# Kernel optimization log

Hardware: AMD Instinct MI355X
Metric: run time of the kernel (lower is better)

Reference implementation:

```python
import jax, jax.numpy as jnp
import numpy as np


def conv2d_nchw(x, w, b, padding):
    # x: [B,Cin,H,W], w: [Cout,Cin,kh,kw]
    y = jax.lax.conv_general_dilated(
        x, w, window_strides=(1, 1), padding=padding,
        dimension_numbers=("NCHW", "OIHW", "NCHW"))
    return y + b[None, :, None, None]


def setup_inputs() -> dict:
    key = jax.random.key(0)
    ks = jax.random.split(key, 8)
    B, C, H, W = 8, 512, 50, 76
    A = 9  # 3 scales x 3 ratios
    base_feat = jax.random.normal(ks[0], (B, C, H, W), dtype=jnp.float32)
    im_info = jnp.tile(jnp.array([800.0, 1216.0, 1.0], jnp.float32), (B, 1))
    gt_boxes = jax.random.uniform(ks[1], (B, 20, 5), dtype=jnp.float32) * 100.0
    num_boxes = jax.random.randint(ks[2], (B,), 1, 20, dtype=jnp.int32)
    # learned parameters (Kaiming-ish small init)
    conv_w = jax.random.normal(ks[3], (512, C, 3, 3), dtype=jnp.float32) * 0.01
    conv_b = jnp.zeros((512,), jnp.float32)
    cls_w = jax.random.normal(ks[4], (2 * A, 512, 1, 1), dtype=jnp.float32) * 0.01
    cls_b = jnp.zeros((2 * A,), jnp.float32)
    bbox_w = jax.random.normal(ks[5], (4 * A, 512, 1, 1), dtype=jnp.float32) * 0.01
    bbox_b = jnp.zeros((4 * A,), jnp.float32)
    return dict(base_feat=base_feat, im_info=im_info, gt_boxes=gt_boxes,
                num_boxes=num_boxes, conv_w=conv_w, conv_b=conv_b,
                cls_w=cls_w, cls_b=cls_b, bbox_w=bbox_w, bbox_b=bbox_b)


def reference(base_feat, im_info, gt_boxes, num_boxes,
              conv_w, conv_b, cls_w, cls_b, bbox_w, bbox_b):
    # RPN_Conv 3x3 + ReLU
    rpn_conv = jax.nn.relu(conv2d_nchw(base_feat, conv_w, conv_b, "SAME"))
    # 1x1 cls head -> [B, 2A, H, W]
    rpn_cls_score = conv2d_nchw(rpn_conv, cls_w, cls_b, "VALID")
    B, C2, H, W = rpn_cls_score.shape
    # _RPN.reshape(x, 2): view as [B, 2, A*H, W], softmax over the 2-way dim
    score_rs = rpn_cls_score.reshape(B, 2, (C2 // 2) * H, W)
    prob_rs = jax.nn.softmax(score_rs, axis=1)
    rpn_cls_prob = prob_rs.reshape(B, C2, H, W)
    # 1x1 bbox head -> [B, 4A, H, W]
    rpn_bbox_pred = conv2d_nchw(rpn_conv, bbox_w, bbox_b, "VALID")
    return rpn_cls_prob, rpn_bbox_pred
```

## Files before the change

kernel.cpp:

```cpp
#include <hip/hip_runtime.h>
#include <hip/hip_bf16.h>


typedef __bf16 bf16_t;
typedef __attribute__((ext_vector_type(8))) __bf16 bf16x8;
typedef __attribute__((ext_vector_type(4))) __bf16 bf16x4;
typedef __attribute__((ext_vector_type(4))) float f32x4;

#define HW 3800
#define NPOS (8 * HW)
#define XP_IMG (52 * 78 * 512)

__device__ __forceinline__ void gload_lds16(const bf16_t* g, char* l) {
  __builtin_amdgcn_global_load_lds(
      (const __attribute__((address_space(1))) unsigned int*)g,
      (__attribute__((address_space(3))) unsigned int*)l, 16, 0, 0);
}

__global__ __launch_bounds__(256) void prep_all(const float* __restrict__ x,
                                                const float* __restrict__ cw,
                                                const float* __restrict__ clsw,
                                                const float* __restrict__ boxw,
                                                bf16_t* __restrict__ Xp,
                                                bf16_t* __restrict__ Wt,
                                                bf16_t* __restrict__ Whb) {
  __shared__ __align__(16) bf16_t tile[76][136];
  __shared__ bf16_t lw[4608];
  const int t = threadIdx.x;
  const int blk = blockIdx.x;
  if (blk < 1600) {
    const int cb = blk & 3;
    int r = blk >> 2;
    const int h = r % 50, b = r / 50;
#pragma unroll
    for (int it = 0; it < 10; ++it) {
      int idx = it * 256 + t;
      if (idx < 2432) {
        int c = idx / 19, w4 = idx - c * 19;
        const float4 v = *(const float4*)(x +
            (((size_t)(b * 512 + cb * 128 + c)) * 50 + h) * 76 + w4 * 4);
        tile[w4 * 4 + 0][c] = (bf16_t)v.x;
        tile[w4 * 4 + 1][c] = (bf16_t)v.y;
        tile[w4 * 4 + 2][c] = (bf16_t)v.z;
        tile[w4 * 4 + 3][c] = (bf16_t)v.w;
      }
    }
    __syncthreads();
#pragma unroll
    for (int it = 0; it < 5; ++it) {
      int idx = it * 256 + t;
      if (idx < 1216) {
        int w = idx >> 4, c8 = idx & 15;
        bf16x8 v = *(const bf16x8*)&tile[w][c8 * 8];
        *(bf16x8*)(Xp + ((size_t)(b * 52 + h + 1) * 78 + (w + 1)) * 512 +
                   cb * 128 + c8 * 8) = v;
      }
    }
  } else if (blk < 1616) {
    const int blk2 = blk - 1600;
    const int b = blk2 >> 1, half = blk2 & 1;
    bf16x8 z;
#pragma unroll
    for (int j = 0; j < 8; ++j) z[j] = (bf16_t)0.f;
#pragma unroll
    for (int it = 0; it < 32; ++it) {
      int idx = it * 256 + t;
      int q = half * 128 + (idx >> 6);
      int c8 = idx & 63;
      int h, w;
      if (q < 78)       { h = 0;           w = q; }
      else if (q < 156) { h = 51;          w = q - 78; }
      else if (q < 206) { h = q - 156 + 1; w = 0; }
      else              { h = q - 206 + 1; w = 77; }
      *(bf16x8*)(Xp + ((size_t)(b * 52 + h) * 78 + w) * 512 + c8 * 8) = z;
    }
  } else if (blk < 2128) {
    const int co = blk - 1616;
    const float* src = cw + (size_t)co * 4608;
#pragma unroll
    for (int it = 0; it < 18; ++it) {
      int idx = it * 256 + t;
      lw[idx] = (bf16_t)src[idx];
    }
    __syncthreads();
#pragma unroll
    for (int s = 0; s < 9; ++s) {
      int ci = t * 2;
      bf16_t v0 = lw[ci * 9 + s], v1 = lw[(ci + 1) * 9 + s];
      bf16_t* dst = Wt + ((size_t)s * 512 + co) * 512 + ci;
      dst[0] = v0; dst[1] = v1;
    }
  } else {
    int g = (blk - 2128) * 256 + t;
    int ci = g & 511; int row = g >> 9;
    float v = 0.f;
    if (row < 18) {
      int a = row >> 1, logit = row & 1;
      v = clsw[(logit * 9 + a) * 512 + ci];
    } else if (row < 54) {
      v = boxw[(row - 18) * 512 + ci];
    }
    Whb[(size_t)row * 512 + ci] = (bf16_t)v;
  }
}

__global__ __launch_bounds__(512) void conv3x3(const bf16_t* __restrict__ Xp,
                                               const bf16_t* __restrict__ Wt,
                                               const float* __restrict__ convb,
                                               bf16_t* __restrict__ rc2) {
  __shared__ __align__(16) char smem[131072];
  const int tid = threadIdx.x;
  const int lane = tid & 63;
  const int wv = tid >> 6;
  const int wm = wv >> 2;
  const int wn = wv & 3;
  const int lm = lane & 15, lg = lane >> 4;

  const int raw = blockIdx.x;
  const int wg = (raw & 7) * 30 + (raw >> 3);
  const int b = wg / 30;
  const int rem = wg - b * 30;
  const int co_base = (rem & 1) * 256;
  const int pos_base = (rem >> 1) * 256;

  int aSrc[4], hB[4], wB[4], cB[4];
#pragma unroll
  for (int i = 0; i < 4; ++i) {
    int d = i * 512 + tid;
    int r = d >> 3, p = d & 7, c = p ^ (r & 7);
    aSrc[i] = (co_base + r) * 512 + c * 8;
    int m = pos_base + r; if (m > HW - 1) m = HW - 1;
    hB[i] = m / 76; wB[i] = m - (m / 76) * 76; cB[i] = c * 8;
  }
  const bf16_t* XpB = Xp + (size_t)b * XP_IMG;

  int aOff[8], bOff[4], koffs[2];
#pragma unroll
  for (int m = 0; m < 8; ++m) aOff[m] = (wm * 128 + m * 16 + lm) * 128;
#pragma unroll
  for (int n = 0; n < 4; ++n) bOff[n] = 32768 + (wn * 64 + n * 16 + lm) * 128;
#pragma unroll
  for (int ks = 0; ks < 2; ++ks) koffs[ks] = ((ks * 4 + lg) ^ (lm & 7)) << 4;

  f32x4 acc[8][4];
#pragma unroll
  for (int i = 0; i < 8; ++i)
#pragma unroll
    for (int j = 0; j < 4; ++j) acc[i][j] = (f32x4){0.f, 0.f, 0.f, 0.f};

#pragma unroll
  for (int i = 0; i < 4; ++i)
    gload_lds16(Wt + aSrc[i], smem + (i * 512 + tid) * 16);
#pragma unroll
  for (int i = 0; i < 4; ++i)
    gload_lds16(XpB + (hB[i] * 78 + wB[i]) * 512 + cB[i],
                smem + 32768 + (i * 512 + tid) * 16);
  asm volatile("s_waitcnt vmcnt(0)" ::: "memory");
  __builtin_amdgcn_s_barrier();
  __builtin_amdgcn_sched_barrier(0);

  for (int kt = 0; kt < 72; ++kt) {
    const int cur = kt & 1;
    const char* Ab = smem + cur * 65536;
    char* Anxt = smem + (cur ^ 1) * 65536;
    const int tn = kt + 1;
    const int sn = tn >> 3, cbn = tn & 7;

    bf16x8 pa[4], pb[4];

    if (tn < 72) {
      const bf16_t* As = Wt + (size_t)sn * 262144 + cbn * 64;
#pragma unroll
      for (int i = 0; i < 4; ++i)
        gload_lds16(As + aSrc[i], Anxt + (i * 512 + tid) * 16);
    }
#pragma unroll
    for (int n = 0; n < 4; ++n) pb[n] = *(const bf16x8*)(Ab + bOff[n] + koffs[0]);
#pragma unroll
    for (int f = 0; f < 4; ++f) pa[f] = *(const bf16x8*)(Ab + aOff[f] + koffs[0]);
    __builtin_amdgcn_s_setprio(1);
#pragma unroll
    for (int f = 0; f < 4; ++f)
#pragma unroll
      for (int n = 0; n < 4; ++n)
        acc[f][n] = __builtin_amdgcn_mfma_f32_16x16x32_bf16(pa[f], pb[n], acc[f][n], 0, 0, 0);
    __builtin_amdgcn_s_setprio(0);
    __builtin_amdgcn_s_barrier();

    if (tn < 72) {
      const int kh = sn / 3, kw = sn - kh * 3;
#pragma unroll
      for (int i = 0; i < 4; ++i) {
        int off = ((hB[i] + kh) * 78 + (wB[i] + kw)) * 512 + cB[i] + cbn * 64;
        gload_lds16(XpB + off, Anxt + 32768 + (i * 512 + tid) * 16);
      }
    }
#pragma unroll
    for (int f = 0; f < 4; ++f) pa[f] = *(const bf16x8*)(Ab + aOff[4 + f] + koffs[0]);
    __builtin_amdgcn_s_setprio(1);
#pragma unroll
    for (int f = 0; f < 4; ++f)
#pragma unroll
      for (int n = 0; n < 4; ++n)
        acc[4 + f][n] = __builtin_amdgcn_mfma_f32_16x16x32_bf16(pa[f], pb[n], acc[4 + f][n], 0, 0, 0);
    __builtin_amdgcn_s_setprio(0);
    __builtin_amdgcn_s_barrier();

#pragma unroll
    for (int n = 0; n < 4; ++n) pb[n] = *(const bf16x8*)(Ab + bOff[n] + koffs[1]);
#pragma unroll
    for (int f = 0; f < 4; ++f) pa[f] = *(const bf16x8*)(Ab + aOff[f] + koffs[1]);
    __builtin_amdgcn_s_setprio(1);
#pragma unroll
    for (int f = 0; f < 4; ++f)
#pragma unroll
      for (int n = 0; n < 4; ++n)
        acc[f][n] = __builtin_amdgcn_mfma_f32_16x16x32_bf16(pa[f], pb[n], acc[f][n], 0, 0, 0);
    __builtin_amdgcn_s_setprio(0);
    __builtin_amdgcn_s_barrier();

#pragma unroll
    for (int f = 0; f < 4; ++f) pa[f] = *(const bf16x8*)(Ab + aOff[4 + f] + koffs[1]);
    __builtin_amdgcn_s_setprio(1);
#pragma unroll
    for (int f = 0; f < 4; ++f)
#pragma unroll
      for (int n = 0; n < 4; ++n)
        acc[4 + f][n] = __builtin_amdgcn_mfma_f32_16x16x32_bf16(pa[f], pb[n], acc[4 + f][n], 0, 0, 0);
    __builtin_amdgcn_s_setprio(0);

    asm volatile("s_waitcnt vmcnt(0)" ::: "memory");
    __builtin_amdgcn_s_barrier();
    __builtin_amdgcn_sched_barrier(0);
  }

  const size_t outRow = (size_t)b * HW;
#pragma unroll
  for (int m = 0; m < 8; ++m) {
    const int co = co_base + wm * 128 + m * 16 + lg * 4;
    const float4 bias = *(const float4*)(convb + co);
#pragma unroll
    for (int n = 0; n < 4; ++n) {
      const int pos = pos_base + wn * 64 + n * 16 + lm;
      if (pos < HW) {
        bf16x4 v;
        float z0 = acc[m][n][0] + bias.x; v[0] = (bf16_t)(z0 > 0.f ? z0 : 0.f);
        float z1 = acc[m][n][1] + bias.y; v[1] = (bf16_t)(z1 > 0.f ? z1 : 0.f);
        float z2 = acc[m][n][2] + bias.z; v[2] = (bf16_t)(z2 > 0.f ? z2 : 0.f);
        float z3 = acc[m][n][3] + bias.w; v[3] = (bf16_t)(z3 > 0.f ? z3 : 0.f);
        *(bf16x4*)(rc2 + (outRow + pos) * 512 + co) = v;
      }
    }
  }
}

__global__ __launch_bounds__(256) void heads_mfma(const bf16_t* __restrict__ rc2,
                                                  const bf16_t* __restrict__ Whb,
                                                  const float* __restrict__ clsb,
                                                  const float* __restrict__ boxb,
                                                  float* __restrict__ out) {
  __shared__ __align__(16) char smem[24576];
  const int t = threadIdx.x, lane = t & 63, wv = t >> 6;
  const int lm = lane & 15, lg = lane >> 4, lx = lane & 7;
  const int pos_base = blockIdx.x * 128;

  int aSrc[2], bSrc[4];
#pragma unroll
  for (int i = 0; i < 2; ++i) {
    int d = i * 256 + t;
    int r = d >> 3, p = d & 7, c = p ^ (r & 7);
    aSrc[i] = r * 512 + c * 8;
  }
#pragma unroll
  for (int i = 0; i < 4; ++i) {
    int d = i * 256 + t;
    int r = d >> 3, p = d & 7, c = p ^ (r & 7);
    int pg = pos_base + r; if (pg > NPOS - 1) pg = NPOS - 1;
    bSrc[i] = pg * 512 + c * 8;
  }

  f32x4 acc[4][2];
#pragma unroll
  for (int i = 0; i < 4; ++i)
#pragma unroll
    for (int j = 0; j < 2; ++j) acc[i][j] = (f32x4){0.f, 0.f, 0.f, 0.f};

  for (int cb = 0; cb < 8; ++cb) {
    __syncthreads();
#pragma unroll
    for (int i = 0; i < 2; ++i) {
      int d = i * 256 + t;
      gload_lds16(Whb + aSrc[i] + cb * 64, &smem[d * 16]);
    }
#pragma unroll
    for (int i = 0; i < 4; ++i) {
      int d = i * 256 + t;
      gload_lds16(rc2 + (size_t)bSrc[i] + cb * 64, &smem[8192 + d * 16]);
    }
    __syncthreads();
#pragma unroll
    for (int ks = 0; ks < 2; ++ks) {
      const int koff = ((ks * 4 + lg) ^ lx) << 4;
      bf16x8 af[4], bfr[2];
#pragma unroll
      for (int f = 0; f < 4; ++f)
        af[f] = *(const bf16x8*)&smem[(f * 16 + lm) * 128 + koff];
#pragma unroll
      for (int f = 0; f < 2; ++f)
        bfr[f] = *(const bf16x8*)&smem[8192 + (wv * 32 + f * 16 + lm) * 128 + koff];
#pragma unroll
      for (int fa = 0; fa < 4; ++fa)
#pragma unroll
        for (int fb = 0; fb < 2; ++fb)
          acc[fa][fb] = __builtin_amdgcn_mfma_f32_16x16x32_bf16(
              af[fa], bfr[fb], acc[fa][fb], 0, 0, 0);
    }
  }

  float* boxOut = out + (size_t)8 * 18 * HW;
#pragma unroll
  for (int fb = 0; fb < 2; ++fb) {
    const int pg = pos_base + wv * 32 + fb * 16 + lm;
    if (pg < NPOS) {
      const int b = pg / HW;
      const int m = pg - b * HW;
#pragma unroll
      for (int fa = 0; fa < 4; ++fa) {
        const int base = fa * 16 + lg * 4;
#pragma unroll
        for (int pr = 0; pr < 2; ++pr) {
          const int row0 = base + pr * 2;
          const float v0 = acc[fa][fb][pr * 2];
          const float v1 = acc[fa][fb][pr * 2 + 1];
          if (row0 < 18) {
            const int a = row0 >> 1;
            const float s0 = v0 + clsb[a];
            const float s1 = v1 + clsb[9 + a];
            const float mx = fmaxf(s0, s1);
            const float e0 = expf(s0 - mx), e1 = expf(s1 - mx);
            const float inv = 1.0f / (e0 + e1);
            out[((size_t)(b * 18 + a)) * HW + m] = e0 * inv;
            out[((size_t)(b * 18 + 9 + a)) * HW + m] = e1 * inv;
          } else if (row0 < 54) {
            const int c0 = row0 - 18;
            boxOut[((size_t)(b * 36 + c0)) * HW + m] = v0 + boxb[c0];
            boxOut[((size_t)(b * 36 + c0 + 1)) * HW + m] = v1 + boxb[c0 + 1];
          }
        }
      }
    }
  }
}

extern "C" void kernel_launch(void* const* d_in, const int* in_sizes, int n_in,
                              void* d_out, int out_size, void* d_ws, size_t ws_size,
                              hipStream_t stream) {
  (void)in_sizes; (void)n_in; (void)out_size; (void)ws_size;
  const float* base_feat = (const float*)d_in[0];
  const float* conv_w = (const float*)d_in[4];
  const float* conv_b = (const float*)d_in[5];
  const float* cls_w  = (const float*)d_in[6];
  const float* cls_b  = (const float*)d_in[7];
  const float* bbox_w = (const float*)d_in[8];
  const float* bbox_b = (const float*)d_in[9];

  char* ws = (char*)d_ws;
  bf16_t* Xp  = (bf16_t*)(ws);
  bf16_t* Wt  = (bf16_t*)(ws + 33226752);
  bf16_t* rc2 = (bf16_t*)(ws + 37945344);
  bf16_t* Whb = (bf16_t*)(ws + 69074944);

  hipLaunchKernelGGL(prep_all,   dim3(2256), dim3(256), 0, stream,
                     base_feat, conv_w, cls_w, bbox_w, Xp, Wt, Whb);
  hipLaunchKernelGGL(conv3x3,    dim3(240),  dim3(512), 0, stream, Xp, Wt, conv_b, rc2);
  hipLaunchKernelGGL(heads_mfma, dim3(238),  dim3(256), 0, stream, rc2, Whb, cls_b, bbox_b,
                     (float*)d_out);
}
```

Before: 158.3 us.

## Fuse 1x1 cls/bbox heads into conv3x3 epilogue with full-Cout tiles

Each conv block now covers all 512 output channels for 128 positions, so the ReLU output tile stays in LDS and the 1x1 head GEMM plus softmax runs in the epilogue. This removes the rc2 intermediate write/read and the separate heads kernel launch. Head weights are pre-packed in MFMA fragment order and read straight from global memory. The K step is halved to 32 with twice the iterations, which means more barriers per FLOP, and the block shape now reloads weights for every position tile.

```diff
diff --git a/kernel.cpp b/kernel.cpp
--- a/kernel.cpp
+++ b/kernel.cpp
@@ -8,7 +8,6 @@
 typedef __attribute__((ext_vector_type(4))) float f32x4;
 
 #define HW 3800
-#define NPOS (8 * HW)
 #define XP_IMG (52 * 78 * 512)
 
 __device__ __forceinline__ void gload_lds16(const bf16_t* g, char* l) {
@@ -23,7 +22,7 @@
                                                 const float* __restrict__ boxw,
                                                 bf16_t* __restrict__ Xp,
                                                 bf16_t* __restrict__ Wt,
-                                                bf16_t* __restrict__ Whb) {
+                                                bf16_t* __restrict__ WhbF) {
   __shared__ __align__(16) bf16_t tile[76][136];
   __shared__ bf16_t lw[4608];
   const int t = threadIdx.x;
@@ -91,56 +90,70 @@
       dst[0] = v0; dst[1] = v1;
     }
   } else {
-    int g = (blk - 2128) * 256 + t;
-    int ci = g & 511; int row = g >> 9;
-    float v = 0.f;
-    if (row < 18) {
-      int a = row >> 1, logit = row & 1;
-      v = clsw[(logit * 9 + a) * 512 + ci];
-    } else if (row < 54) {
-      v = boxw[(row - 18) * 512 + ci];
-    }
-    Whb[(size_t)row * 512 + ci] = (bf16_t)v;
+    int idx = (blk - 2128) * 256 + t;
+    int lane = idx & 63, kt = (idx >> 6) & 15, mf = idx >> 10;
+    int row = mf * 16 + (lane & 15);
+    int ci0 = kt * 32 + (lane >> 4) * 8;
+    bf16x8 v;
+#pragma unroll
+    for (int j = 0; j < 8; ++j) {
+      float val = 0.f;
+      if (row < 18) {
+        int a = row >> 1, logit = row & 1;
+        val = clsw[(logit * 9 + a) * 512 + ci0 + j];
+      } else if (row < 54) {
+        val = boxw[(row - 18) * 512 + ci0 + j];
+      }
+      v[j] = (bf16_t)val;
+    }
+    *(bf16x8*)(WhbF + (size_t)idx * 8) = v;
   }
 }
 
-__global__ __launch_bounds__(512) void conv3x3(const bf16_t* __restrict__ Xp,
-                                               const bf16_t* __restrict__ Wt,
-                                               const float* __restrict__ convb,
-                                               bf16_t* __restrict__ rc2) {
+__global__ __launch_bounds__(512) void conv_fused(const bf16_t* __restrict__ Xp,
+                                                  const bf16_t* __restrict__ Wt,
+                                                  const float* __restrict__ convb,
+                                                  const bf16_t* __restrict__ WhbF,
+                                                  const float* __restrict__ clsb,
+                                                  const float* __restrict__ boxb,
+                                                  float* __restrict__ out) {
   __shared__ __align__(16) char smem[131072];
   const int tid = threadIdx.x;
   const int lane = tid & 63;
   const int wv = tid >> 6;
-  const int wm = wv >> 2;
-  const int wn = wv & 3;
+  const int wm = wv >> 1;
+  const int wn = wv & 1;
   const int lm = lane & 15, lg = lane >> 4;
 
   const int raw = blockIdx.x;
   const int wg = (raw & 7) * 30 + (raw >> 3);
   const int b = wg / 30;
-  const int rem = wg - b * 30;
-  const int co_base = (rem & 1) * 256;
-  const int pos_base = (rem >> 1) * 256;
-
-  int aSrc[4], hB[4], wB[4], cB[4];
+  const int pos_base = (wg - b * 30) * 128;
+  const bf16_t* XpB = Xp + (size_t)b * XP_IMG;
+
+  int aSrc[4], aDst[4];
 #pragma unroll
   for (int i = 0; i < 4; ++i) {
     int d = i * 512 + tid;
-    int r = d >> 3, p = d & 7, c = p ^ (r & 7);
-    aSrc[i] = (co_base + r) * 512 + c * 8;
+    int r = d >> 2, p = d & 3, c = p ^ ((r >> 1) & 3);
+    aSrc[i] = r * 512 + c * 8;
+    aDst[i] = r * 64 + p * 16;
+  }
+  int bSpa, bCc, bDst;
+  {
+    int r = tid >> 2, p = tid & 3, c = p ^ ((r >> 1) & 3);
     int m = pos_base + r; if (m > HW - 1) m = HW - 1;
-    hB[i] = m / 76; wB[i] = m - (m / 76) * 76; cB[i] = c * 8;
-  }
-  const bf16_t* XpB = Xp + (size_t)b * XP_IMG;
-
-  int aOff[8], bOff[4], koffs[2];
-#pragma unroll
-  for (int m = 0; m < 8; ++m) aOff[m] = (wm * 128 + m * 16 + lm) * 128;
-#pragma unroll
-  for (int n = 0; n < 4; ++n) bOff[n] = 32768 + (wn * 64 + n * 16 + lm) * 128;
-#pragma unroll
-  for (int ks = 0; ks < 2; ++ks) koffs[ks] = ((ks * 4 + lg) ^ (lm & 7)) << 4;
+    bSpa = (m / 76) * 78 + (m - (m / 76) * 76);
+    bCc = c * 8;
+    bDst = 32768 + r * 64 + p * 16;
+  }
+
+  const int koff = (lg ^ ((lm >> 1) & 3)) << 4;
+  int aOff[8], bOff[4];
+#pragma unroll
+  for (int m = 0; m < 8; ++m) aOff[m] = (wm * 128 + m * 16 + lm) * 64 + koff;
+#pragma unroll
+  for (int n = 0; n < 4; ++n) bOff[n] = 32768 + (wn * 64 + n * 16 + lm) * 64 + koff;
 
   f32x4 acc[8][4];
 #pragma unroll
@@ -148,36 +161,37 @@
 #pragma unroll
     for (int j = 0; j < 4; ++j) acc[i][j] = (f32x4){0.f, 0.f, 0.f, 0.f};
 
-#pragma unroll
-  for (int i = 0; i < 4; ++i)
-    gload_lds16(Wt + aSrc[i], smem + (i * 512 + tid) * 16);
-#pragma unroll
-  for (int i = 0; i < 4; ++i)
-    gload_lds16(XpB + (hB[i] * 78 + wB[i]) * 512 + cB[i],
-                smem + 32768 + (i * 512 + tid) * 16);
+#define STAGE_A(KT, BUF) {                                                      \
+    const int s_ = (KT) >> 4, cb_ = (KT) & 15;                                  \
+    const bf16_t* p_ = Wt + (size_t)s_ * 262144 + cb_ * 32;                     \
+    _Pragma("unroll")                                                           \
+    for (int i_ = 0; i_ < 4; ++i_)                                              \
+      gload_lds16(p_ + aSrc[i_], (BUF) + aDst[i_]);                             \
+  }
+#define STAGE_B(KT, BUF) {                                                      \
+    const int s_ = (KT) >> 4, cb_ = (KT) & 15;                                  \
+    const int sp_ = (s_ / 3) * 78 + (s_ - (s_ / 3) * 3);                        \
+    gload_lds16(XpB + (size_t)(bSpa + sp_) * 512 + bCc + cb_ * 32,              \
+                (BUF) + bDst);                                                  \
+  }
+
+  STAGE_A(0, smem)
+  STAGE_B(0, smem)
   asm volatile("s_waitcnt vmcnt(0)" ::: "memory");
   __builtin_amdgcn_s_barrier();
   __builtin_amdgcn_sched_barrier(0);
 
-  for (int kt = 0; kt < 72; ++kt) {
-    const int cur = kt & 1;
-    const char* Ab = smem + cur * 65536;
-    char* Anxt = smem + (cur ^ 1) * 65536;
+  for (int kt = 0; kt < 144; ++kt) {
+    const char* Ab = smem + (kt & 1) * 40960;
+    char* Anxt = smem + ((kt + 1) & 1) * 40960;
     const int tn = kt + 1;
-    const int sn = tn >> 3, cbn = tn & 7;
-
     bf16x8 pa[4], pb[4];
 
-    if (tn < 72) {
-      const bf16_t* As = Wt + (size_t)sn * 262144 + cbn * 64;
-#pragma unroll
-      for (int i = 0; i < 4; ++i)
-        gload_lds16(As + aSrc[i], Anxt + (i * 512 + tid) * 16);
-    }
-#pragma unroll
-    for (int n = 0; n < 4; ++n) pb[n] = *(const bf16x8*)(Ab + bOff[n] + koffs[0]);
-#pragma unroll
-    for (int f = 0; f < 4; ++f) pa[f] = *(const bf16x8*)(Ab + aOff[f] + koffs[0]);
+    if (tn < 144) STAGE_A(tn, Anxt)
+#pragma unroll
+    for (int n = 0; n < 4; ++n) pb[n] = *(const bf16x8*)(Ab + bOff[n]);
+#pragma unroll
+    for (int f = 0; f < 4; ++f) pa[f] = *(const bf16x8*)(Ab + aOff[f]);
     __builtin_amdgcn_s_setprio(1);
 #pragma unroll
     for (int f = 0; f < 4; ++f)
@@ -187,16 +201,9 @@
     __builtin_amdgcn_s_setprio(0);
     __builtin_amdgcn_s_barrier();
 
-    if (tn < 72) {
-      const int kh = sn / 3, kw = sn - kh * 3;
-#pragma unroll
-      for (int i = 0; i < 4; ++i) {
-        int off = ((hB[i] + kh) * 78 + (wB[i] + kw)) * 512 + cB[i] + cbn * 64;
-        gload_lds16(XpB + off, Anxt + 32768 + (i * 512 + tid) * 16);
-      }
-    }
-#pragma unroll
-    for (int f = 0; f < 4; ++f) pa[f] = *(const bf16x8*)(Ab + aOff[4 + f] + koffs[0]);
+    if (tn < 144) STAGE_B(tn, Anxt)
+#pragma unroll
+    for (int f = 0; f < 4; ++f) pa[f] = *(const bf16x8*)(Ab + aOff[4 + f]);
     __builtin_amdgcn_s_setprio(1);
 #pragma unroll
     for (int f = 0; f < 4; ++f)
@@ -204,134 +211,60 @@
       for (int n = 0; n < 4; ++n)
         acc[4 + f][n] = __builtin_amdgcn_mfma_f32_16x16x32_bf16(pa[f], pb[n], acc[4 + f][n], 0, 0, 0);
     __builtin_amdgcn_s_setprio(0);
-    __builtin_amdgcn_s_barrier();
-
-#pragma unroll
-    for (int n = 0; n < 4; ++n) pb[n] = *(const bf16x8*)(Ab + bOff[n] + koffs[1]);
-#pragma unroll
-    for (int f = 0; f < 4; ++f) pa[f] = *(const bf16x8*)(Ab + aOff[f] + koffs[1]);
-    __builtin_amdgcn_s_setprio(1);
-#pragma unroll
-    for (int f = 0; f < 4; ++f)
-#pragma unroll
-      for (int n = 0; n < 4; ++n)
-        acc[f][n] = __builtin_amdgcn_mfma_f32_16x16x32_bf16(pa[f], pb[n], acc[f][n], 0, 0, 0);
-    __builtin_amdgcn_s_setprio(0);
-    __builtin_amdgcn_s_barrier();
-
-#pragma unroll
-    for (int f = 0; f < 4; ++f) pa[f] = *(const bf16x8*)(Ab + aOff[4 + f] + koffs[1]);
-    __builtin_amdgcn_s_setprio(1);
-#pragma unroll
-    for (int f = 0; f < 4; ++f)
-#pragma unroll
-      for (int n = 0; n < 4; ++n)
-        acc[4 + f][n] = __builtin_amdgcn_mfma_f32_16x16x32_bf16(pa[f], pb[n], acc[4 + f][n], 0, 0, 0);
-    __builtin_amdgcn_s_setprio(0);
 
     asm volatile("s_waitcnt vmcnt(0)" ::: "memory");
     __builtin_amdgcn_s_barrier();
     __builtin_amdgcn_sched_barrier(0);
   }
-
-  const size_t outRow = (size_t)b * HW;
+#undef STAGE_A
+#undef STAGE_B
+
 #pragma unroll
   for (int m = 0; m < 8; ++m) {
-    const int co = co_base + wm * 128 + m * 16 + lg * 4;
+    const int co = wm * 128 + m * 16 + lg * 4;
     const float4 bias = *(const float4*)(convb + co);
+    const int cb2 = co * 2;
 #pragma unroll
     for (int n = 0; n < 4; ++n) {
-      const int pos = pos_base + wn * 64 + n * 16 + lm;
-      if (pos < HW) {
-        bf16x4 v;
-        float z0 = acc[m][n][0] + bias.x; v[0] = (bf16_t)(z0 > 0.f ? z0 : 0.f);
-        float z1 = acc[m][n][1] + bias.y; v[1] = (bf16_t)(z1 > 0.f ? z1 : 0.f);
-        float z2 = acc[m][n][2] + bias.z; v[2] = (bf16_t)(z2 > 0.f ? z2 : 0.f);
-        float z3 = acc[m][n][3] + bias.w; v[3] = (bf16_t)(z3 > 0.f ? z3 : 0.f);
-        *(bf16x4*)(rc2 + (outRow + pos) * 512 + co) = v;
-      }
-    }
-  }
-}
-
-__global__ __launch_bounds__(256) void heads_mfma(const bf16_t* __restrict__ rc2,
-                                                  const bf16_t* __restrict__ Whb,
-                                                  const float* __restrict__ clsb,
-                                                  const float* __restrict__ boxb,
-                                                  float* __restrict__ out) {
-  __shared__ __align__(16) char smem[24576];
-  const int t = threadIdx.x, lane = t & 63, wv = t >> 6;
-  const int lm = lane & 15, lg = lane >> 4, lx = lane & 7;
-  const int pos_base = blockIdx.x * 128;
-
-  int aSrc[2], bSrc[4];
-#pragma unroll
-  for (int i = 0; i < 2; ++i) {
-    int d = i * 256 + t;
-    int r = d >> 3, p = d & 7, c = p ^ (r & 7);
-    aSrc[i] = r * 512 + c * 8;
-  }
-#pragma unroll
-  for (int i = 0; i < 4; ++i) {
-    int d = i * 256 + t;
-    int r = d >> 3, p = d & 7, c = p ^ (r & 7);
-    int pg = pos_base + r; if (pg > NPOS - 1) pg = NPOS - 1;
-    bSrc[i] = pg * 512 + c * 8;
-  }
-
-  f32x4 acc[4][2];
-#pragma unroll
-  for (int i = 0; i < 4; ++i)
-#pragma unroll
-    for (int j = 0; j < 2; ++j) acc[i][j] = (f32x4){0.f, 0.f, 0.f, 0.f};
-
-  for (int cb = 0; cb < 8; ++cb) {
-    __syncthreads();
-#pragma unroll
-    for (int i = 0; i < 2; ++i) {
-      int d = i * 256 + t;
-      gload_lds16(Whb + aSrc[i] + cb * 64, &smem[d * 16]);
-    }
-#pragma unroll
-    for (int i = 0; i < 4; ++i) {
-      int d = i * 256 + t;
-      gload_lds16(rc2 + (size_t)bSrc[i] + cb * 64, &smem[8192 + d * 16]);
-    }
-    __syncthreads();
-#pragma unroll
-    for (int ks = 0; ks < 2; ++ks) {
-      const int koff = ((ks * 4 + lg) ^ lx) << 4;
-      bf16x8 af[4], bfr[2];
-#pragma unroll
-      for (int f = 0; f < 4; ++f)
-        af[f] = *(const bf16x8*)&smem[(f * 16 + lm) * 128 + koff];
-#pragma unroll
-      for (int f = 0; f < 2; ++f)
-        bfr[f] = *(const bf16x8*)&smem[8192 + (wv * 32 + f * 16 + lm) * 128 + koff];
-#pragma unroll
-      for (int fa = 0; fa < 4; ++fa)
-#pragma unroll
-        for (int fb = 0; fb < 2; ++fb)
-          acc[fa][fb] = __builtin_amdgcn_mfma_f32_16x16x32_bf16(
-              af[fa], bfr[fb], acc[fa][fb], 0, 0, 0);
-    }
-  }
-
-  float* boxOut = out + (size_t)8 * 18 * HW;
-#pragma unroll
-  for (int fb = 0; fb < 2; ++fb) {
-    const int pg = pos_base + wv * 32 + fb * 16 + lm;
-    if (pg < NPOS) {
-      const int b = pg / HW;
-      const int m = pg - b * HW;
-#pragma unroll
-      for (int fa = 0; fa < 4; ++fa) {
-        const int base = fa * 16 + lg * 4;
+      const int pl = wn * 64 + n * 16 + lm;
+      bf16x4 v;
+      float z0 = acc[m][n][0] + bias.x; v[0] = (bf16_t)(z0 > 0.f ? z0 : 0.f);
+      float z1 = acc[m][n][1] + bias.y; v[1] = (bf16_t)(z1 > 0.f ? z1 : 0.f);
+      float z2 = acc[m][n][2] + bias.z; v[2] = (bf16_t)(z2 > 0.f ? z2 : 0.f);
+      float z3 = acc[m][n][3] + bias.w; v[3] = (bf16_t)(z3 > 0.f ? z3 : 0.f);
+      *(bf16x4*)(smem + pl * 1024 + (cb2 ^ ((pl & 7) << 4))) = v;
+    }
+  }
+  __syncthreads();
+
+  {
+    const int ps = wv * 16;
+    const int prow = ps + lm;
+    const int rsw = (lm & 7) << 4;
+    f32x4 acc2[4];
+#pragma unroll
+    for (int i = 0; i < 4; ++i) acc2[i] = (f32x4){0.f, 0.f, 0.f, 0.f};
+#pragma unroll
+    for (int kt = 0; kt < 16; ++kt) {
+      const bf16x8 bfr = *(const bf16x8*)(smem + prow * 1024 +
+                                          ((kt * 64 + lg * 16) ^ rsw));
+#pragma unroll
+      for (int mf = 0; mf < 4; ++mf) {
+        const bf16x8 af = *(const bf16x8*)(WhbF +
+            ((size_t)(mf * 16 + kt) * 64 + lane) * 8);
+        acc2[mf] = __builtin_amdgcn_mfma_f32_16x16x32_bf16(af, bfr, acc2[mf], 0, 0, 0);
+      }
+    }
+    const int pos = pos_base + ps + lm;
+    if (pos < HW) {
+      float* boxOut = out + (size_t)8 * 18 * HW;
+#pragma unroll
+      for (int mf = 0; mf < 4; ++mf) {
 #pragma unroll
         for (int pr = 0; pr < 2; ++pr) {
-          const int row0 = base + pr * 2;
-          const float v0 = acc[fa][fb][pr * 2];
-          const float v1 = acc[fa][fb][pr * 2 + 1];
+          const int row0 = mf * 16 + lg * 4 + pr * 2;
+          const float v0 = acc2[mf][pr * 2];
+          const float v1 = acc2[mf][pr * 2 + 1];
           if (row0 < 18) {
             const int a = row0 >> 1;
             const float s0 = v0 + clsb[a];
@@ -339,12 +272,12 @@
             const float mx = fmaxf(s0, s1);
             const float e0 = expf(s0 - mx), e1 = expf(s1 - mx);
             const float inv = 1.0f / (e0 + e1);
-            out[((size_t)(b * 18 + a)) * HW + m] = e0 * inv;
-            out[((size_t)(b * 18 + 9 + a)) * HW + m] = e1 * inv;
+            out[((size_t)(b * 18 + a)) * HW + pos] = e0 * inv;
+            out[((size_t)(b * 18 + 9 + a)) * HW + pos] = e1 * inv;
           } else if (row0 < 54) {
             const int c0 = row0 - 18;
-            boxOut[((size_t)(b * 36 + c0)) * HW + m] = v0 + boxb[c0];
-            boxOut[((size_t)(b * 36 + c0 + 1)) * HW + m] = v1 + boxb[c0 + 1];
+            boxOut[((size_t)(b * 36 + c0)) * HW + pos] = v0 + boxb[c0];
+            boxOut[((size_t)(b * 36 + c0 + 1)) * HW + pos] = v1 + boxb[c0 + 1];
           }
         }
       }
@@ -365,14 +298,12 @@
   const float* bbox_b = (const float*)d_in[9];
 
   char* ws = (char*)d_ws;
-  bf16_t* Xp  = (bf16_t*)(ws);
-  bf16_t* Wt  = (bf16_t*)(ws + 33226752);
-  bf16_t* rc2 = (bf16_t*)(ws + 37945344);
-  bf16_t* Whb = (bf16_t*)(ws + 69074944);
-
-  hipLaunchKernelGGL(prep_all,   dim3(2256), dim3(256), 0, stream,
-                     base_feat, conv_w, cls_w, bbox_w, Xp, Wt, Whb);
-  hipLaunchKernelGGL(conv3x3,    dim3(240),  dim3(512), 0, stream, Xp, Wt, conv_b, rc2);
-  hipLaunchKernelGGL(heads_mfma, dim3(238),  dim3(256), 0, stream, rc2, Whb, cls_b, bbox_b,
-                     (float*)d_out);
+  bf16_t* Xp   = (bf16_t*)(ws);
+  bf16_t* Wt   = (bf16_t*)(ws + 33226752);
+  bf16_t* WhbF = (bf16_t*)(ws + 37945344);
+
+  hipLaunchKernelGGL(prep_all,   dim3(2144), dim3(256), 0, stream,
+                     base_feat, conv_w, cls_w, bbox_w, Xp, Wt, WhbF);
+  hipLaunchKernelGGL(conv_fused, dim3(240),  dim3(512), 0, stream,
+                     Xp, Wt, conv_b, WhbF, cls_b, bbox_b, (float*)d_out);
 }
```

New measurement: 163.4 us. +3.3%, slower.

## Shrink conv3x3 tile to 256x128 with K=32 steps and two blocks per CU

Applied to the files above, without the earlier changes.

The implicit-GEMM conv3x3 block drops from 512 threads with a 256x256 output tile and K=64 per stage to 256 threads with a 256x128 tile and K=32 per stage. LDS use falls from 128 KB to 48 KB, the XOR swizzle changes to suit 64-byte rows, and the grid doubles to 480 blocks with launch_bounds(256,2). The aim is to fill all CUs on the MI355X (240 blocks left some idle) and let two blocks share a CU to hide latency. In exchange, each block reuses its weight tile across fewer positions, runs twice as many K iterations with a barrier each, and so spends more on synchronisation and global loads.

```diff
diff --git a/kernel.cpp b/kernel.cpp
--- a/kernel.cpp
+++ b/kernel.cpp
@@ -104,43 +104,51 @@
   }
 }
 
-__global__ __launch_bounds__(512) void conv3x3(const bf16_t* __restrict__ Xp,
-                                               const bf16_t* __restrict__ Wt,
-                                               const float* __restrict__ convb,
-                                               bf16_t* __restrict__ rc2) {
-  __shared__ __align__(16) char smem[131072];
+__global__ __launch_bounds__(256, 2) void conv3x3(const bf16_t* __restrict__ Xp,
+                                                  const bf16_t* __restrict__ Wt,
+                                                  const float* __restrict__ convb,
+                                                  bf16_t* __restrict__ rc2) {
+  __shared__ __align__(16) char smem[49152];
   const int tid = threadIdx.x;
   const int lane = tid & 63;
   const int wv = tid >> 6;
-  const int wm = wv >> 2;
-  const int wn = wv & 3;
+  const int wm = wv >> 1;
+  const int wn = wv & 1;
   const int lm = lane & 15, lg = lane >> 4;
 
   const int raw = blockIdx.x;
-  const int wg = (raw & 7) * 30 + (raw >> 3);
-  const int b = wg / 30;
-  const int rem = wg - b * 30;
+  const int wg = (raw & 7) * 60 + (raw >> 3);
+  const int b = wg / 60;
+  const int rem = wg - b * 60;
   const int co_base = (rem & 1) * 256;
-  const int pos_base = (rem >> 1) * 256;
-
-  int aSrc[4], hB[4], wB[4], cB[4];
+  const int pos_base = (rem >> 1) * 128;
+  const bf16_t* XpB = Xp + (size_t)b * XP_IMG;
+
+  int aSrc[4], aDst[4];
 #pragma unroll
   for (int i = 0; i < 4; ++i) {
-    int d = i * 512 + tid;
-    int r = d >> 3, p = d & 7, c = p ^ (r & 7);
+    int d = i * 256 + tid;
+    int r = d >> 2, p = d & 3, c = p ^ ((r >> 1) & 3);
     aSrc[i] = (co_base + r) * 512 + c * 8;
+    aDst[i] = r * 64 + p * 16;
+  }
+  int bSpa[2], bCc[2], bDst[2];
+#pragma unroll
+  for (int i = 0; i < 2; ++i) {
+    int d = i * 256 + tid;
+    int r = d >> 2, p = d & 3, c = p ^ ((r >> 1) & 3);
     int m = pos_base + r; if (m > HW - 1) m = HW - 1;
-    hB[i] = m / 76; wB[i] = m - (m / 76) * 76; cB[i] = c * 8;
-  }
-  const bf16_t* XpB = Xp + (size_t)b * XP_IMG;
-
-  int aOff[8], bOff[4], koffs[2];
-#pragma unroll
-  for (int m = 0; m < 8; ++m) aOff[m] = (wm * 128 + m * 16 + lm) * 128;
-#pragma unroll
-  for (int n = 0; n < 4; ++n) bOff[n] = 32768 + (wn * 64 + n * 16 + lm) * 128;
-#pragma unroll
-  for (int ks = 0; ks < 2; ++ks) koffs[ks] = ((ks * 4 + lg) ^ (lm & 7)) << 4;
+    bSpa[i] = (m / 76) * 78 + (m - (m / 76) * 76);
+    bCc[i] = c * 8;
+    bDst[i] = 16384 + r * 64 + p * 16;
+  }
+
+  const int koff = (lg ^ ((lm >> 1) & 3)) << 4;
+  int aOff[8], bOff[4];
+#pragma unroll
+  for (int m = 0; m < 8; ++m) aOff[m] = (wm * 128 + m * 16 + lm) * 64 + koff;
+#pragma unroll
+  for (int n = 0; n < 4; ++n) bOff[n] = 16384 + (wn * 64 + n * 16 + lm) * 64 + koff;
 
   f32x4 acc[8][4];
 #pragma unroll
@@ -148,36 +156,40 @@
 #pragma unroll
     for (int j = 0; j < 4; ++j) acc[i][j] = (f32x4){0.f, 0.f, 0.f, 0.f};
 
-#pragma unroll
-  for (int i = 0; i < 4; ++i)
-    gload_lds16(Wt + aSrc[i], smem + (i * 512 + tid) * 16);
-#pragma unroll
-  for (int i = 0; i < 4; ++i)
-    gload_lds16(XpB + (hB[i] * 78 + wB[i]) * 512 + cB[i],
-                smem + 32768 + (i * 512 + tid) * 16);
+#define STAGE_A(KT, BUF) {                                                      \
+    const int s_ = (KT) >> 4, cb_ = (KT) & 15;                                  \
+    const bf16_t* p_ = Wt + (size_t)s_ * 262144 + cb_ * 32;                     \
+    _Pragma("unroll")                                                           \
+    for (int i_ = 0; i_ < 4; ++i_)                                              \
+      gload_lds16(p_ + aSrc[i_], (BUF) + aDst[i_]);                             \
+  }
+#define STAGE_B(KT, BUF) {                                                      \
+    const int s_ = (KT) >> 4, cb_ = (KT) & 15;                                  \
+    const int sp_ = (s_ / 3) * 78 + (s_ - (s_ / 3) * 3);                        \
+    _Pragma("unroll")                                                           \
+    for (int i_ = 0; i_ < 2; ++i_)                                              \
+      gload_lds16(XpB + (size_t)(bSpa[i_] + sp_) * 512 + bCc[i_] + cb_ * 32,    \
+                  (BUF) + bDst[i_]);                                            \
+  }
+
+  STAGE_A(0, smem)
+  STAGE_B(0, smem)
   asm volatile("s_waitcnt vmcnt(0)" ::: "memory");
   __builtin_amdgcn_s_barrier();
   __builtin_amdgcn_sched_barrier(0);
 
-  for (int kt = 0; kt < 72; ++kt) {
-    const int cur = kt & 1;
-    const char* Ab = smem + cur * 65536;
-    char* Anxt = smem + (cur ^ 1) * 65536;
+  for (int kt = 0; kt < 144; ++kt) {
+    const char* Ab = smem + (kt & 1) * 24576;
+    char* Anxt = smem + ((kt + 1) & 1) * 24576;
     const int tn = kt + 1;
-    const int sn = tn >> 3, cbn = tn & 7;
-
+    const bool more = (tn < 144);
     bf16x8 pa[4], pb[4];
 
-    if (tn < 72) {
-      const bf16_t* As = Wt + (size_t)sn * 262144 + cbn * 64;
-#pragma unroll
-      for (int i = 0; i < 4; ++i)
-        gload_lds16(As + aSrc[i], Anxt + (i * 512 + tid) * 16);
-    }
-#pragma unroll
-    for (int n = 0; n < 4; ++n) pb[n] = *(const bf16x8*)(Ab + bOff[n] + koffs[0]);
-#pragma unroll
-    for (int f = 0; f < 4; ++f) pa[f] = *(const bf16x8*)(Ab + aOff[f] + koffs[0]);
+    if (more) STAGE_A(tn, Anxt)
+#pragma unroll
+    for (int n = 0; n < 4; ++n) pb[n] = *(const bf16x8*)(Ab + bOff[n]);
+#pragma unroll
+    for (int f = 0; f < 4; ++f) pa[f] = *(const bf16x8*)(Ab + aOff[f]);
     __builtin_amdgcn_s_setprio(1);
 #pragma unroll
     for (int f = 0; f < 4; ++f)
@@ -187,16 +199,9 @@
     __builtin_amdgcn_s_setprio(0);
     __builtin_amdgcn_s_barrier();
 
-    if (tn < 72) {
-      const int kh = sn / 3, kw = sn - kh * 3;
-#pragma unroll
-      for (int i = 0; i < 4; ++i) {
-        int off = ((hB[i] + kh) * 78 + (wB[i] + kw)) * 512 + cB[i] + cbn * 64;
-        gload_lds16(XpB + off, Anxt + 32768 + (i * 512 + tid) * 16);
-      }
-    }
-#pragma unroll
-    for (int f = 0; f < 4; ++f) pa[f] = *(const bf16x8*)(Ab + aOff[4 + f] + koffs[0]);
+    if (more) STAGE_B(tn, Anxt)
+#pragma unroll
+    for (int f = 0; f < 4; ++f) pa[f] = *(const bf16x8*)(Ab + aOff[4 + f]);
     __builtin_amdgcn_s_setprio(1);
 #pragma unroll
     for (int f = 0; f < 4; ++f)
@@ -204,35 +209,13 @@
       for (int n = 0; n < 4; ++n)
         acc[4 + f][n] = __builtin_amdgcn_mfma_f32_16x16x32_bf16(pa[f], pb[n], acc[4 + f][n], 0, 0, 0);
     __builtin_amdgcn_s_setprio(0);
-    __builtin_amdgcn_s_barrier();
-
-#pragma unroll
-    for (int n = 0; n < 4; ++n) pb[n] = *(const bf16x8*)(Ab + bOff[n] + koffs[1]);
-#pragma unroll
-    for (int f = 0; f < 4; ++f) pa[f] = *(const bf16x8*)(Ab + aOff[f] + koffs[1]);
-    __builtin_amdgcn_s_setprio(1);
-#pragma unroll
-    for (int f = 0; f < 4; ++f)
-#pragma unroll
-      for (int n = 0; n < 4; ++n)
-        acc[f][n] = __builtin_amdgcn_mfma_f32_16x16x32_bf16(pa[f], pb[n], acc[f][n], 0, 0, 0);
-    __builtin_amdgcn_s_setprio(0);
-    __builtin_amdgcn_s_barrier();
-
-#pragma unroll
-    for (int f = 0; f < 4; ++f) pa[f] = *(const bf16x8*)(Ab + aOff[4 + f] + koffs[1]);
-    __builtin_amdgcn_s_setprio(1);
-#pragma unroll
-    for (int f = 0; f < 4; ++f)
-#pragma unroll
-      for (int n = 0; n < 4; ++n)
-        acc[4 + f][n] = __builtin_amdgcn_mfma_f32_16x16x32_bf16(pa[f], pb[n], acc[4 + f][n], 0, 0, 0);
-    __builtin_amdgcn_s_setprio(0);
 
     asm volatile("s_waitcnt vmcnt(0)" ::: "memory");
     __builtin_amdgcn_s_barrier();
     __builtin_amdgcn_sched_barrier(0);
   }
+#undef STAGE_A
+#undef STAGE_B
 
   const size_t outRow = (size_t)b * HW;
 #pragma unroll
@@ -372,7 +355,7 @@
 
   hipLaunchKernelGGL(prep_all,   dim3(2256), dim3(256), 0, stream,
                      base_feat, conv_w, cls_w, bbox_w, Xp, Wt, Whb);
-  hipLaunchKernelGGL(conv3x3,    dim3(240),  dim3(512), 0, stream, Xp, Wt, conv_b, rc2);
+  hipLaunchKernelGGL(conv3x3,    dim3(480),  dim3(256), 0, stream, Xp, Wt, conv_b, rc2);
   hipLaunchKernelGGL(heads_mfma, dim3(238),  dim3(256), 0, stream, rc2, Whb, cls_b, bbox_b,
                      (float*)d_out);
 }
```

Result: slower. 176.4 us (+11.5%).
